# Performance work log

Measured on AMD Instinct MI355X. Metric: run time of the kernel, lower is better.

The kernel has to match this reference:

```python
import jax, jax.numpy as jnp
import numpy as np

B, T, N_EMBD, HEAD = 8, 2048, 1024, 64

def setup_inputs() -> dict:
    key = jax.random.key(0)
    kx, kk, kq, kv = jax.random.split(key, 4)
    x = jax.random.normal(kx, (B, T, N_EMBD), dtype=jnp.float32)
    Wk = jax.random.normal(kk, (HEAD, N_EMBD), dtype=jnp.float32) * 0.02
    Wq = jax.random.normal(kq, (HEAD, N_EMBD), dtype=jnp.float32) * 0.02
    Wv = jax.random.normal(kv, (HEAD, N_EMBD), dtype=jnp.float32) * 0.02
    return {"x": x, "Wk": Wk, "Wq": Wq, "Wv": Wv}

def reference(x, Wk, Wq, Wv):
    # x: [B, T, C]; Linear(n_embd, head_size, bias=False) => x @ W.T
    Bq, Tq, C = x.shape
    q = jnp.einsum('btc,hc->bth', x, Wq)  # [B, T, H]
    k = jnp.einsum('btc,hc->bth', x, Wk)
    v = jnp.einsum('btc,hc->bth', x, Wv)
    # NOTE: source scales by C**0.5 with C = n_embd (not head_size); preserved.
    scale = 1.0 / jnp.sqrt(jnp.float32(C))
    wei = jnp.einsum('bth,bsh->bts', q, k) * scale  # [B, T, T]
    # causal mask: allow key position s <= query position t
    causal = jnp.tril(jnp.ones((Tq, Tq), dtype=bool))
    wei = jnp.where(causal[None, :, :], wei, -jnp.inf)
    wei = jax.nn.softmax(wei, axis=-1)
    # dropout is identity at inference
    out = jnp.einsum('bts,bsh->bth', wei, v)  # [B, T, H]
    return out
```

## Files before the change

kernel.cpp:

```cpp
#include <hip/hip_runtime.h>

#define TB 2048
#define NB 8
#define CEMB 1024
#define HD 64
#define BT (NB*TB)
#define QSCALE 0.04508422f

typedef __attribute__((ext_vector_type(8))) short bf16x8;
typedef __attribute__((ext_vector_type(4))) short bf16x4;
typedef __attribute__((ext_vector_type(4))) float f32x4;

#define MFMA32(a, b, c) __builtin_amdgcn_mfma_f32_16x16x32_bf16(a, b, c, 0, 0, 0)
#define MFMA16(a, b, c) __builtin_amdgcn_mfma_f32_16x16x16bf16_1k(a, b, c, 0, 0, 0)

__device__ inline short f2bf(float f) {
    union { float f; unsigned u; } v; v.f = f;
    unsigned r = v.u + 0x7fffu + ((v.u >> 16) & 1u);
    return (short)(r >> 16);
}
__device__ inline float bf2f(short s) {
    union { unsigned u; float f; } v; v.u = ((unsigned)(unsigned short)s) << 16;
    return v.f;
}
__device__ inline unsigned cvt_pk_bf16(float a, float b) {
    unsigned r;
    asm("v_cvt_pk_bf16_f32 %0, %1, %2" : "=v"(r) : "v"(a), "v"(b));
    return r;
}
__device__ inline bf16x4 pack2(unsigned w0, unsigned w1) {
    union { unsigned u[2]; bf16x4 v; } c; c.u[0] = w0; c.u[1] = w1; return c.v;
}
__device__ inline bf16x8 pack4(unsigned w0, unsigned w1, unsigned w2, unsigned w3) {
    union { unsigned u[4]; bf16x8 v; } c;
    c.u[0] = w0; c.u[1] = w1; c.u[2] = w2; c.u[3] = w3; return c.v;
}
__device__ inline float bflo(unsigned w) {
    union { unsigned u; float f; } v; v.u = w << 16; return v.f;
}
__device__ inline float bfhi(unsigned w) {
    union { unsigned u; float f; } v; v.u = w & 0xffff0000u; return v.f;
}

__global__ __launch_bounds__(256) void wpack(const float* __restrict__ Wk,
                                             const float* __restrict__ Wq,
                                             const float* __restrict__ Wv,
                                             short* __restrict__ W2) {
    int c = blockIdx.x * 256 + threadIdx.x;
    int lane = c & 63, ntk = c >> 6;
    int nt = ntk % 12, kc = ntk / 12;
    int n = nt * 16 + (lane & 15);
    int col = kc * 32 + (lane >> 4) * 8;
    const float* src = (n < 64) ? Wk + n * 1024
                     : (n < 128) ? Wq + (n - 64) * 1024
                                 : Wv + (n - 128) * 1024;
    float4 a = *(const float4*)(src + col);
    float4 b = *(const float4*)(src + col + 4);
    bf16x8 o;
    o[0] = f2bf(a.x); o[1] = f2bf(a.y); o[2] = f2bf(a.z); o[3] = f2bf(a.w);
    o[4] = f2bf(b.x); o[5] = f2bf(b.y); o[6] = f2bf(b.z); o[7] = f2bf(b.w);
    *(bf16x8*)(W2 + (size_t)c * 8) = o;
}

__global__ __launch_bounds__(256) void qkv_proj(const float* __restrict__ x,
                                                const short* __restrict__ W2,
                                                short* __restrict__ Qb,
                                                short* __restrict__ Kb,
                                                short* __restrict__ Vt) {
    __shared__ uint2 Lred[4][3][6][64];
    int tid = threadIdx.x, wave = tid >> 6, lane = tid & 63;
    int l15 = lane & 15, quad = lane >> 4;
    int m0 = blockIdx.x * 32;

    f32x4 acc[24];
#pragma unroll
    for (int i = 0; i < 24; ++i) acc[i] = f32x4{0.f, 0.f, 0.f, 0.f};

    const float4* xA = (const float4*)(x + (size_t)(m0 + l15) * CEMB + wave * 256) + quad * 2;
    const float4* xB = (const float4*)(x + (size_t)(m0 + 16 + l15) * CEMB + wave * 256) + quad * 2;
    float4 xq[8];
    xq[0] = xA[0]; xq[1] = xA[1]; xq[2] = xB[0]; xq[3] = xB[1];
    xq[4] = xA[8]; xq[5] = xA[9]; xq[6] = xB[8]; xq[7] = xB[9];

    const short* wbase = W2 + ((size_t)(wave * 8) * 12 * 64 + lane) * 8;
#pragma unroll
    for (int kc = 0; kc < 8; ++kc) {
        bf16x8 wf[12];
#pragma unroll
        for (int nt = 0; nt < 12; ++nt)
            wf[nt] = *(const bf16x8*)(wbase + (size_t)kc * 6144 + nt * 512);
        int base = (kc & 1) * 4;
        float4 a0 = xq[base], a1 = xq[base + 1];
        float4 b0 = xq[base + 2], b1 = xq[base + 3];
        if (kc + 2 < 8) {
            xq[base]     = xA[(kc + 2) * 8]; xq[base + 1] = xA[(kc + 2) * 8 + 1];
            xq[base + 2] = xB[(kc + 2) * 8]; xq[base + 3] = xB[(kc + 2) * 8 + 1];
        }
        bf16x8 af0, af1;
        af0[0] = f2bf(a0.x); af0[1] = f2bf(a0.y); af0[2] = f2bf(a0.z); af0[3] = f2bf(a0.w);
        af0[4] = f2bf(a1.x); af0[5] = f2bf(a1.y); af0[6] = f2bf(a1.z); af0[7] = f2bf(a1.w);
        af1[0] = f2bf(b0.x); af1[1] = f2bf(b0.y); af1[2] = f2bf(b0.z); af1[3] = f2bf(b0.w);
        af1[4] = f2bf(b1.x); af1[5] = f2bf(b1.y); af1[6] = f2bf(b1.z); af1[7] = f2bf(b1.w);
#pragma unroll
        for (int nt = 0; nt < 12; ++nt) {
            acc[nt * 2]     = MFMA32(af0, wf[nt], acc[nt * 2]);
            acc[nt * 2 + 1] = MFMA32(af1, wf[nt], acc[nt * 2 + 1]);
        }
    }

#pragma unroll
    for (int nt = 0; nt < 12; ++nt) {
#pragma unroll
        for (int mt = 0; mt < 2; ++mt) {
            int o = nt / 3;
            if (o != wave) {
                int rank = wave - (wave > o ? 1 : 0);
                uint2 p;
                p.x = cvt_pk_bf16(acc[nt * 2 + mt][0], acc[nt * 2 + mt][1]);
                p.y = cvt_pk_bf16(acc[nt * 2 + mt][2], acc[nt * 2 + mt][3]);
                Lred[o][rank][(nt % 3) * 2 + mt][lane] = p;
            }
        }
    }
    __syncthreads();

    int b = blockIdx.x >> 6;
    int sblk32 = blockIdx.x & 63;
#pragma unroll
    for (int nt = 0; nt < 12; ++nt) {
        if (wave == nt / 3) {
            f32x4 s0 = acc[nt * 2], s1 = acc[nt * 2 + 1];
#pragma unroll
            for (int rk = 0; rk < 3; ++rk) {
                uint2 p0 = Lred[nt / 3][rk][(nt % 3) * 2][lane];
                uint2 p1 = Lred[nt / 3][rk][(nt % 3) * 2 + 1][lane];
                s0[0] += bflo(p0.x); s0[1] += bfhi(p0.x); s0[2] += bflo(p0.y); s0[3] += bfhi(p0.y);
                s1[0] += bflo(p1.x); s1[1] += bfhi(p1.x); s1[2] += bflo(p1.y); s1[3] += bfhi(p1.y);
            }
            if (nt < 4) {
                int h = nt * 16 + l15;
#pragma unroll
                for (int r = 0; r < 4; ++r) {
                    Kb[(size_t)(m0 + quad * 4 + r) * HD + h]      = f2bf(s0[r]);
                    Kb[(size_t)(m0 + 16 + quad * 4 + r) * HD + h] = f2bf(s1[r]);
                }
            } else if (nt < 8) {
                int h = (nt - 4) * 16 + l15;
#pragma unroll
                for (int r = 0; r < 4; ++r) {
                    Qb[(size_t)(m0 + quad * 4 + r) * HD + h]      = f2bf(s0[r] * QSCALE);
                    Qb[(size_t)(m0 + 16 + quad * 4 + r) * HD + h] = f2bf(s1[r] * QSCALE);
                }
            } else {
                int h = (nt - 8) * 16 + l15;
                bf16x8 v8 = pack4(cvt_pk_bf16(s0[0], s0[1]), cvt_pk_bf16(s0[2], s0[3]),
                                  cvt_pk_bf16(s1[0], s1[1]), cvt_pk_bf16(s1[2], s1[3]));
                *(bf16x8*)(Vt + ((size_t)((b * 64 + sblk32) * 64 + h)) * 32 + quad * 8) = v8;
            }
        }
    }
}

__global__ __launch_bounds__(256) void flash(const short* __restrict__ Qb,
                                             const short* __restrict__ Kb,
                                             const short* __restrict__ Vt,
                                             float* __restrict__ out) {
    __shared__ float Of[4][2][16][68];
    __shared__ float Ml[4][2][16];
    int tid = threadIdx.x, wave = tid >> 6, lane = tid & 63;
    int l15 = lane & 15, quad = lane >> 4;
    int i = blockIdx.x;
    int round = i >> 8, s = i & 255;
    int b = s & 7;
    int g32 = s >> 3;
    int q32 = round ? 63 - g32 : g32;
    int tq0 = q32 * 32;
    size_t bT = (size_t)b * TB;

    const short* qr0 = Qb + (bT + tq0 + l15) * HD;
    const short* qr1 = Qb + (bT + tq0 + 16 + l15) * HD;
    bf16x8 qf00 = *(const bf16x8*)(qr0 + quad * 8);
    bf16x8 qf01 = *(const bf16x8*)(qr0 + 32 + quad * 8);
    bf16x8 qf10 = *(const bf16x8*)(qr1 + quad * 8);
    bf16x8 qf11 = *(const bf16x8*)(qr1 + 32 + quad * 8);

    bf16x4 ones4;
#pragma unroll
    for (int j = 0; j < 4; ++j) ones4[j] = (short)0x3F80;

    f32x4 accO0[4], accO1[4];
#pragma unroll
    for (int k = 0; k < 4; ++k) { accO0[k] = f32x4{0.f,0.f,0.f,0.f}; accO1[k] = f32x4{0.f,0.f,0.f,0.f}; }
    f32x4 accL0 = f32x4{0.f,0.f,0.f,0.f}, accL1 = f32x4{0.f,0.f,0.f,0.f};

    int ntiles = (tq0 + 95) >> 6;
    const short* kbase = Kb + bT * HD;
    const short* vtb = Vt + (size_t)b * 131072;

    int myt = wave;
    if (myt < ntiles) {
        bf16x8 kf[8];
        {
            const short* kr = kbase + (size_t)(myt * 64 + l15) * HD + quad * 8;
#pragma unroll
            for (int st = 0; st < 4; ++st) {
                kf[st * 2]     = *(const bf16x8*)(kr + (size_t)st * 16 * HD);
                kf[st * 2 + 1] = *(const bf16x8*)(kr + (size_t)st * 16 * HD + 32);
            }
        }
        for (; myt < ntiles; myt += 4) {
            int s0 = myt * 64;
            bf16x8 vf8[8];
#pragma unroll
            for (int sb2 = 0; sb2 < 2; ++sb2)
#pragma unroll
                for (int ht = 0; ht < 4; ++ht)
                    vf8[sb2 * 4 + ht] = *(const bf16x8*)(
                        vtb + ((size_t)(((s0 >> 5) + sb2) * 64 + ht * 16 + l15)) * 32 + quad * 8);
            f32x4 sv0[4], sv1[4];
#pragma unroll
            for (int st = 0; st < 4; ++st) {
                f32x4 t0 = f32x4{0.f,0.f,0.f,0.f}, t1 = f32x4{0.f,0.f,0.f,0.f};
                t0 = MFMA32(kf[st * 2], qf00, t0);
                t0 = MFMA32(kf[st * 2 + 1], qf01, t0);
                t1 = MFMA32(kf[st * 2], qf10, t1);
                t1 = MFMA32(kf[st * 2 + 1], qf11, t1);
                sv0[st] = t0; sv1[st] = t1;
            }
            if (myt + 4 < ntiles) {
                const short* kr = kbase + (size_t)(s0 + 256 + l15) * HD + quad * 8;
#pragma unroll
                for (int st = 0; st < 4; ++st) {
                    kf[st * 2]     = *(const bf16x8*)(kr + (size_t)st * 16 * HD);
                    kf[st * 2 + 1] = *(const bf16x8*)(kr + (size_t)st * 16 * HD + 32);
                }
            }
            bf16x4 pk0[4], pk1[4];
            if (s0 + 63 <= tq0) {
#pragma unroll
                for (int st = 0; st < 4; ++st) {
                    unsigned w00 = cvt_pk_bf16(__builtin_amdgcn_exp2f(sv0[st][0]),
                                               __builtin_amdgcn_exp2f(sv0[st][1]));
                    unsigned w01 = cvt_pk_bf16(__builtin_amdgcn_exp2f(sv0[st][2]),
                                               __builtin_amdgcn_exp2f(sv0[st][3]));
                    unsigned w10 = cvt_pk_bf16(__builtin_amdgcn_exp2f(sv1[st][0]),
                                               __builtin_amdgcn_exp2f(sv1[st][1]));
                    unsigned w11 = cvt_pk_bf16(__builtin_amdgcn_exp2f(sv1[st][2]),
                                               __builtin_amdgcn_exp2f(sv1[st][3]));
                    pk0[st] = pack2(w00, w01);
                    pk1[st] = pack2(w10, w11);
                }
            } else {
                int t0g = tq0 + l15, t1g = tq0 + 16 + l15;
#pragma unroll
                for (int st = 0; st < 4; ++st) {
                    bool full0 = (s0 + st * 16 + 15 <= tq0);
                    bool full1 = (s0 + st * 16 + 15 <= tq0 + 16);
                    int sb = s0 + st * 16 + quad * 4;
                    float a0 = (full0 || sb + 0 <= t0g) ? __builtin_amdgcn_exp2f(sv0[st][0]) : 0.f;
                    float a1 = (full0 || sb + 1 <= t0g) ? __builtin_amdgcn_exp2f(sv0[st][1]) : 0.f;
                    float a2 = (full0 || sb + 2 <= t0g) ? __builtin_amdgcn_exp2f(sv0[st][2]) : 0.f;
                    float a3 = (full0 || sb + 3 <= t0g) ? __builtin_amdgcn_exp2f(sv0[st][3]) : 0.f;
                    float c0 = (full1 || sb + 0 <= t1g) ? __builtin_amdgcn_exp2f(sv1[st][0]) : 0.f;
                    float c1 = (full1 || sb + 1 <= t1g) ? __builtin_amdgcn_exp2f(sv1[st][1]) : 0.f;
                    float c2 = (full1 || sb + 2 <= t1g) ? __builtin_amdgcn_exp2f(sv1[st][2]) : 0.f;
                    float c3 = (full1 || sb + 3 <= t1g) ? __builtin_amdgcn_exp2f(sv1[st][3]) : 0.f;
                    pk0[st] = pack2(cvt_pk_bf16(a0, a1), cvt_pk_bf16(a2, a3));
                    pk1[st] = pack2(cvt_pk_bf16(c0, c1), cvt_pk_bf16(c2, c3));
                }
            }
#pragma unroll
            for (int g = 0; g < 4; ++g) {
                accL0 = MFMA16(ones4, pk0[g], accL0);
                accL1 = MFMA16(ones4, pk1[g], accL1);
#pragma unroll
                for (int ht = 0; ht < 4; ++ht) {
                    bf16x8 v = vf8[(g >> 1) * 4 + ht];
                    bf16x4 va;
                    if (g & 1) { va[0] = v[4]; va[1] = v[5]; va[2] = v[6]; va[3] = v[7]; }
                    else       { va[0] = v[0]; va[1] = v[1]; va[2] = v[2]; va[3] = v[3]; }
                    accO0[ht] = MFMA16(va, pk0[g], accO0[ht]);
                    accO1[ht] = MFMA16(va, pk1[g], accO1[ht]);
                }
            }
        }
    }

#pragma unroll
    for (int ht = 0; ht < 4; ++ht) {
        float4 o0, o1;
        o0.x = accO0[ht][0]; o0.y = accO0[ht][1]; o0.z = accO0[ht][2]; o0.w = accO0[ht][3];
        o1.x = accO1[ht][0]; o1.y = accO1[ht][1]; o1.z = accO1[ht][2]; o1.w = accO1[ht][3];
        *(float4*)&Of[wave][0][l15][ht * 16 + quad * 4] = o0;
        *(float4*)&Of[wave][1][l15][ht * 16 + quad * 4] = o1;
    }
    if (quad == 0) { Ml[wave][0][l15] = accL0[0]; Ml[wave][1][l15] = accL1[0]; }
    __syncthreads();

    int row = tid >> 4, c4 = (tid & 15) * 4;
#pragma unroll
    for (int qt = 0; qt < 2; ++qt) {
        float L = Ml[0][qt][row] + Ml[1][qt][row] + Ml[2][qt][row] + Ml[3][qt][row];
        float inv = 1.0f / L;
        float4 p0 = *(const float4*)&Of[0][qt][row][c4];
        float4 p1 = *(const float4*)&Of[1][qt][row][c4];
        float4 p2 = *(const float4*)&Of[2][qt][row][c4];
        float4 p3 = *(const float4*)&Of[3][qt][row][c4];
        float4 o;
        o.x = (p0.x + p1.x + p2.x + p3.x) * inv;
        o.y = (p0.y + p1.y + p2.y + p3.y) * inv;
        o.z = (p0.z + p1.z + p2.z + p3.z) * inv;
        o.w = (p0.w + p1.w + p2.w + p3.w) * inv;
        *(float4*)(out + (bT + tq0 + qt * 16 + row) * HD + c4) = o;
    }
}

extern "C" void kernel_launch(void* const* d_in, const int* in_sizes, int n_in,
                              void* d_out, int out_size, void* d_ws, size_t ws_size,
                              hipStream_t stream) {
    const float* x  = (const float*)d_in[0];
    const float* Wk = (const float*)d_in[1];
    const float* Wq = (const float*)d_in[2];
    const float* Wv = (const float*)d_in[3];
    float* out = (float*)d_out;

    short* W2 = (short*)d_ws;
    short* Qb = W2 + 192 * 1024;
    short* Kb = Qb + (size_t)BT * HD;
    short* Vt = Kb + (size_t)BT * HD;

    wpack<<<96, 256, 0, stream>>>(Wk, Wq, Wv, W2);
    qkv_proj<<<512, 256, 0, stream>>>(x, W2, Qb, Kb, Vt);
    flash<<<512, 256, 0, stream>>>(Qb, Kb, Vt, out);
}
```

Before: 141.5 us.

## Halve qkv_proj rows per block, add occupancy hint, prioritize MFMA in flash

The QKV projection now processes 16 rows per block instead of 32 and launches 1024 blocks. This halves its accumulator registers and LDS reduction buffer, and a launch_bounds occupancy hint of 4 is added. V-transposed stores become half-width writes at an offset chosen by block parity. The flash kernel wraps its MFMA sections in s_setprio so matrix work gets issue priority over other waves. The cost is that each W2 fragment load is now reused across half as many rows, so weight traffic goes up.

Measured after the change: 134.3 us. -5.1%, faster.

```diff
diff --git a/kernel.cpp b/kernel.cpp
--- a/kernel.cpp
+++ b/kernel.cpp
@@ -62,25 +62,23 @@
     *(bf16x8*)(W2 + (size_t)c * 8) = o;
 }
 
-__global__ __launch_bounds__(256) void qkv_proj(const float* __restrict__ x,
-                                                const short* __restrict__ W2,
-                                                short* __restrict__ Qb,
-                                                short* __restrict__ Kb,
-                                                short* __restrict__ Vt) {
-    __shared__ uint2 Lred[4][3][6][64];
+__global__ __launch_bounds__(256, 4) void qkv_proj(const float* __restrict__ x,
+                                                   const short* __restrict__ W2,
+                                                   short* __restrict__ Qb,
+                                                   short* __restrict__ Kb,
+                                                   short* __restrict__ Vt) {
+    __shared__ uint2 Lred[4][3][3][64];
     int tid = threadIdx.x, wave = tid >> 6, lane = tid & 63;
     int l15 = lane & 15, quad = lane >> 4;
-    int m0 = blockIdx.x * 32;
-
-    f32x4 acc[24];
-#pragma unroll
-    for (int i = 0; i < 24; ++i) acc[i] = f32x4{0.f, 0.f, 0.f, 0.f};
+    int m0 = blockIdx.x * 16;
+
+    f32x4 acc[12];
+#pragma unroll
+    for (int i = 0; i < 12; ++i) acc[i] = f32x4{0.f, 0.f, 0.f, 0.f};
 
     const float4* xA = (const float4*)(x + (size_t)(m0 + l15) * CEMB + wave * 256) + quad * 2;
-    const float4* xB = (const float4*)(x + (size_t)(m0 + 16 + l15) * CEMB + wave * 256) + quad * 2;
-    float4 xq[8];
-    xq[0] = xA[0]; xq[1] = xA[1]; xq[2] = xB[0]; xq[3] = xB[1];
-    xq[4] = xA[8]; xq[5] = xA[9]; xq[6] = xB[8]; xq[7] = xB[9];
+    float4 xq[4];
+    xq[0] = xA[0]; xq[1] = xA[1]; xq[2] = xA[8]; xq[3] = xA[9];
 
     const short* wbase = W2 + ((size_t)(wave * 8) * 12 * 64 + lane) * 8;
 #pragma unroll
@@ -89,73 +87,62 @@
 #pragma unroll
         for (int nt = 0; nt < 12; ++nt)
             wf[nt] = *(const bf16x8*)(wbase + (size_t)kc * 6144 + nt * 512);
-        int base = (kc & 1) * 4;
+        int base = (kc & 1) * 2;
         float4 a0 = xq[base], a1 = xq[base + 1];
-        float4 b0 = xq[base + 2], b1 = xq[base + 3];
         if (kc + 2 < 8) {
-            xq[base]     = xA[(kc + 2) * 8]; xq[base + 1] = xA[(kc + 2) * 8 + 1];
-            xq[base + 2] = xB[(kc + 2) * 8]; xq[base + 3] = xB[(kc + 2) * 8 + 1];
-        }
-        bf16x8 af0, af1;
-        af0[0] = f2bf(a0.x); af0[1] = f2bf(a0.y); af0[2] = f2bf(a0.z); af0[3] = f2bf(a0.w);
-        af0[4] = f2bf(a1.x); af0[5] = f2bf(a1.y); af0[6] = f2bf(a1.z); af0[7] = f2bf(a1.w);
-        af1[0] = f2bf(b0.x); af1[1] = f2bf(b0.y); af1[2] = f2bf(b0.z); af1[3] = f2bf(b0.w);
-        af1[4] = f2bf(b1.x); af1[5] = f2bf(b1.y); af1[6] = f2bf(b1.z); af1[7] = f2bf(b1.w);
-#pragma unroll
-        for (int nt = 0; nt < 12; ++nt) {
-            acc[nt * 2]     = MFMA32(af0, wf[nt], acc[nt * 2]);
-            acc[nt * 2 + 1] = MFMA32(af1, wf[nt], acc[nt * 2 + 1]);
-        }
+            xq[base]     = xA[(kc + 2) * 8];
+            xq[base + 1] = xA[(kc + 2) * 8 + 1];
+        }
+        bf16x8 af0 = pack4(cvt_pk_bf16(a0.x, a0.y), cvt_pk_bf16(a0.z, a0.w),
+                           cvt_pk_bf16(a1.x, a1.y), cvt_pk_bf16(a1.z, a1.w));
+#pragma unroll
+        for (int nt = 0; nt < 12; ++nt)
+            acc[nt] = MFMA32(af0, wf[nt], acc[nt]);
     }
 
 #pragma unroll
     for (int nt = 0; nt < 12; ++nt) {
-#pragma unroll
-        for (int mt = 0; mt < 2; ++mt) {
-            int o = nt / 3;
-            if (o != wave) {
-                int rank = wave - (wave > o ? 1 : 0);
-                uint2 p;
-                p.x = cvt_pk_bf16(acc[nt * 2 + mt][0], acc[nt * 2 + mt][1]);
-                p.y = cvt_pk_bf16(acc[nt * 2 + mt][2], acc[nt * 2 + mt][3]);
-                Lred[o][rank][(nt % 3) * 2 + mt][lane] = p;
-            }
+        int o = nt / 3;
+        if (o != wave) {
+            int rank = wave - (wave > o ? 1 : 0);
+            uint2 p;
+            p.x = cvt_pk_bf16(acc[nt][0], acc[nt][1]);
+            p.y = cvt_pk_bf16(acc[nt][2], acc[nt][3]);
+            Lred[o][rank][nt % 3][lane] = p;
         }
     }
     __syncthreads();
 
-    int b = blockIdx.x >> 6;
-    int sblk32 = blockIdx.x & 63;
+    int b = blockIdx.x >> 7;
+    int sblk32 = (blockIdx.x & 127) >> 1;
+    int half = blockIdx.x & 1;
 #pragma unroll
     for (int nt = 0; nt < 12; ++nt) {
         if (wave == nt / 3) {
-            f32x4 s0 = acc[nt * 2], s1 = acc[nt * 2 + 1];
+            f32x4 s0 = acc[nt];
 #pragma unroll
             for (int rk = 0; rk < 3; ++rk) {
-                uint2 p0 = Lred[nt / 3][rk][(nt % 3) * 2][lane];
-                uint2 p1 = Lred[nt / 3][rk][(nt % 3) * 2 + 1][lane];
-                s0[0] += bflo(p0.x); s0[1] += bfhi(p0.x); s0[2] += bflo(p0.y); s0[3] += bfhi(p0.y);
-                s1[0] += bflo(p1.x); s1[1] += bfhi(p1.x); s1[2] += bflo(p1.y); s1[3] += bfhi(p1.y);
+                uint2 p0 = Lred[nt / 3][rk][nt % 3][lane];
+                s0[0] += bflo(p0.x); s0[1] += bfhi(p0.x);
+                s0[2] += bflo(p0.y); s0[3] += bfhi(p0.y);
             }
             if (nt < 4) {
                 int h = nt * 16 + l15;
 #pragma unroll
-                for (int r = 0; r < 4; ++r) {
-                    Kb[(size_t)(m0 + quad * 4 + r) * HD + h]      = f2bf(s0[r]);
-                    Kb[(size_t)(m0 + 16 + quad * 4 + r) * HD + h] = f2bf(s1[r]);
-                }
+                for (int r = 0; r < 4; ++r)
+                    Kb[(size_t)(m0 + quad * 4 + r) * HD + h] = f2bf(s0[r]);
             } else if (nt < 8) {
                 int h = (nt - 4) * 16 + l15;
 #pragma unroll
-                for (int r = 0; r < 4; ++r) {
-                    Qb[(size_t)(m0 + quad * 4 + r) * HD + h]      = f2bf(s0[r] * QSCALE);
-                    Qb[(size_t)(m0 + 16 + quad * 4 + r) * HD + h] = f2bf(s1[r] * QSCALE);
-                }
+                for (int r = 0; r < 4; ++r)
+                    Qb[(size_t)(m0 + quad * 4 + r) * HD + h] = f2bf(s0[r] * QSCALE);
             } else {
                 int h = (nt - 8) * 16 + l15;
-                bf16x8 v8 = pack4(cvt_pk_bf16(s0[0], s0[1]), cvt_pk_bf16(s0[2], s0[3]),
-                                  cvt_pk_bf16(s1[0], s1[1]), cvt_pk_bf16(s1[2], s1[3]));
-                *(bf16x8*)(Vt + ((size_t)((b * 64 + sblk32) * 64 + h)) * 32 + quad * 8) = v8;
+                uint2 v2;
+                v2.x = cvt_pk_bf16(s0[0], s0[1]);
+                v2.y = cvt_pk_bf16(s0[2], s0[3]);
+                *(uint2*)(Vt + ((size_t)((b * 64 + sblk32) * 64 + h)) * 32
+                             + quad * 8 + half * 4) = v2;
             }
         }
     }
@@ -218,6 +205,7 @@
                     vf8[sb2 * 4 + ht] = *(const bf16x8*)(
                         vtb + ((size_t)(((s0 >> 5) + sb2) * 64 + ht * 16 + l15)) * 32 + quad * 8);
             f32x4 sv0[4], sv1[4];
+            __builtin_amdgcn_s_setprio(1);
 #pragma unroll
             for (int st = 0; st < 4; ++st) {
                 f32x4 t0 = f32x4{0.f,0.f,0.f,0.f}, t1 = f32x4{0.f,0.f,0.f,0.f};
@@ -227,6 +215,7 @@
                 t1 = MFMA32(kf[st * 2 + 1], qf11, t1);
                 sv0[st] = t0; sv1[st] = t1;
             }
+            __builtin_amdgcn_s_setprio(0);
             if (myt + 4 < ntiles) {
                 const short* kr = kbase + (size_t)(s0 + 256 + l15) * HD + quad * 8;
 #pragma unroll
@@ -269,6 +258,7 @@
                     pk1[st] = pack2(cvt_pk_bf16(c0, c1), cvt_pk_bf16(c2, c3));
                 }
             }
+            __builtin_amdgcn_s_setprio(1);
 #pragma unroll
             for (int g = 0; g < 4; ++g) {
                 accL0 = MFMA16(ones4, pk0[g], accL0);
@@ -283,6 +273,7 @@
                     accO1[ht] = MFMA16(va, pk1[g], accO1[ht]);
                 }
             }
+            __builtin_amdgcn_s_setprio(0);
         }
     }
 
@@ -330,6 +321,6 @@
     short* Vt = Kb + (size_t)BT * HD;
 
     wpack<<<96, 256, 0, stream>>>(Wk, Wq, Wv, W2);
-    qkv_proj<<<512, 256, 0, stream>>>(x, W2, Qb, Kb, Vt);
+    qkv_proj<<<1024, 256, 0, stream>>>(x, W2, Qb, Kb, Vt);
     flash<<<512, 256, 0, stream>>>(Qb, Kb, Vt, out);
 }
```
